# Kernel tuning notes

Measured on AMD Instinct MI355X. Metric: run time of the kernel, lower is better.

The kernel has to match this reference:

```python
import jax, jax.numpy as jnp
import numpy as np

DIM, HEADS, WH, WW, NPROMPT, NW, BATCH = 384, 12, 7, 7, 5, 64, 32
N = WH * WW + NPROMPT  # 54


def _make_rel_index():
    ch, cw = np.meshgrid(np.arange(WH), np.arange(WW), indexing='ij')
    coords = np.stack([ch, cw]).reshape(2, -1)  # [2, 49]
    rel = coords[:, :, None] - coords[:, None, :]  # [2,49,49]
    rel = rel.transpose(1, 2, 0)
    rel[:, :, 0] += WH - 1
    rel[:, :, 1] += WW - 1
    rel[:, :, 0] *= 2 * WW - 1
    return rel.sum(-1).astype(np.int32)  # [49,49]


def setup_inputs() -> dict:
    key = jax.random.key(0)
    ks = jax.random.split(key, 7)
    B_ = BATCH * NW
    x = jax.random.normal(ks[0], (B_, N, DIM), jnp.float32)
    # 0/-inf style shifted-window mask; random floats exercise the same math
    mask = jnp.where(jax.random.uniform(ks[1], (NW, WH * WW, WH * WW)) > 0.8,
                     jnp.float32(-100.0), jnp.float32(0.0))
    qkv_w = 0.02 * jax.random.normal(ks[2], (3 * DIM, DIM), jnp.float32)
    qkv_b = 0.02 * jax.random.normal(ks[3], (3 * DIM,), jnp.float32)
    proj_w = 0.02 * jax.random.normal(ks[4], (DIM, DIM), jnp.float32)
    proj_b = 0.02 * jax.random.normal(ks[5], (DIM,), jnp.float32)
    rpb_table = 0.02 * jax.random.normal(ks[6], ((2 * WH - 1) * (2 * WW - 1), HEADS), jnp.float32)
    rel_index = jnp.asarray(_make_rel_index())
    return {"x": x, "mask": mask, "qkv_w": qkv_w, "qkv_b": qkv_b,
            "proj_w": proj_w, "proj_b": proj_b, "rpb_table": rpb_table,
            "rel_index": rel_index}


def reference(x, mask, qkv_w, qkv_b, proj_w, proj_b, rpb_table, rel_index):
    B_, n, C = x.shape
    hd = C // HEADS
    scale = hd ** -0.5
    qkv = (x @ qkv_w.T + qkv_b).reshape(B_, n, 3, HEADS, hd)
    qkv = jnp.moveaxis(qkv, 2, 0)  # [3, B_, n, H, hd]
    q, k, v = qkv[0], qkv[1], qkv[2]  # [B_, n, H, hd]
    attn = jnp.einsum('bnhd,bmhd->bhnm', q * scale, k)  # [B_, H, n, n]
    nw2 = WH * WW
    bias = rpb_table[rel_index.reshape(-1)].reshape(nw2, nw2, HEADS)
    bias = jnp.transpose(bias, (2, 0, 1))  # [H, 49, 49]
    bias = jnp.pad(bias, ((0, 0), (NPROMPT, 0), (NPROMPT, 0)))  # [H, n, n]
    attn = attn + bias[None]
    nW = mask.shape[0]
    mask_p = jnp.pad(mask, ((0, 0), (NPROMPT, 0), (NPROMPT, 0)))  # [nW, n, n]
    attn = attn.reshape(B_ // nW, nW, HEADS, n, n) + mask_p[None, :, None]
    attn = jax.nn.softmax(attn.reshape(B_, HEADS, n, n), axis=-1)
    out = jnp.einsum('bhnm,bmhd->bnhd', attn, v).reshape(B_, n, C)
    return out @ proj_w.T + proj_b
```

## Files before the change

kernel.cpp:

```cpp
#include <hip/hip_runtime.h>

#define DIM 384
#define NH 12
#define NT 54
#define NWIN 64

typedef __attribute__((ext_vector_type(8))) short short8;
typedef __attribute__((ext_vector_type(4))) float f32x4;

__device__ __forceinline__ unsigned short f2bf(float f) {
  unsigned int u = __float_as_uint(f);
  u += 0x7fffu + ((u >> 16) & 1u);
  return (unsigned short)(u >> 16);
}
__device__ __forceinline__ float bf2f(unsigned short s) {
  return __uint_as_float((unsigned int)s << 16);
}

__global__ __launch_bounds__(256) void convert_x(
    const float* __restrict__ x, unsigned short* __restrict__ xb) {
  const size_t i8 = ((size_t)blockIdx.x * 256 + threadIdx.x) * 8;
  float4 fa = *(const float4*)&x[i8];
  float4 fb = *(const float4*)&x[i8 + 4];
  short8 s;
  s[0] = f2bf(fa.x); s[1] = f2bf(fa.y); s[2] = f2bf(fa.z); s[3] = f2bf(fa.w);
  s[4] = f2bf(fb.x); s[5] = f2bf(fb.y); s[6] = f2bf(fb.z); s[7] = f2bf(fb.w);
  *(short8*)&xb[i8] = s;
}

__global__ __launch_bounds__(256) void prep2_kernel(
    const float* __restrict__ qkv_w, const float* __restrict__ proj_w,
    const float* __restrict__ mask, const float* __restrict__ rpb,
    const int* __restrict__ rel,
    unsigned short* __restrict__ Wq, unsigned short* __restrict__ Wp,
    unsigned short* __restrict__ bmt) {
  int idx = blockIdx.x * 256 + threadIdx.x;
  if (idx < 1152 * 384) { Wq[idx] = f2bf(qkv_w[idx]); return; }
  idx -= 1152 * 384;
  if (idx < 384 * 384) { Wp[idx] = f2bf(proj_w[idx]); return; }
  idx -= 384 * 384;
  if (idx < NWIN * NH * 64 * 64) {
    int w = idx / (NH * 4096);
    int rem = idx - w * (NH * 4096);
    int h = rem >> 12, r = (rem >> 6) & 63, c = rem & 63;
    float v;
    if (r >= NT || c >= NT) v = -1e30f;
    else if (r >= 5 && c >= 5)
      v = rpb[rel[(r - 5) * 49 + (c - 5)] * NH + h] +
          mask[w * 2401 + (r - 5) * 49 + (c - 5)];
    else v = 0.0f;
    bmt[w * (NH * 4096) + rem] = f2bf(v);
  }
}

__global__ __launch_bounds__(256) void qkv_gemm2(
    const unsigned short* __restrict__ xb, const unsigned short* __restrict__ Wq,
    const float* __restrict__ qkv_b, unsigned short* __restrict__ QKVb) {
  __shared__ unsigned short As[128][72];
  __shared__ unsigned short Bs[128][72];
  const int tid = threadIdx.x;
  const int n0 = blockIdx.x * 128;
  const size_t m0 = (size_t)blockIdx.y * 128;
  const int wv = tid >> 6, ln = tid & 63, g = ln >> 4, lc = ln & 15;
  const int wr = (wv >> 1) * 64, wc = (wv & 1) * 64;
  f32x4 acc[4][4];
#pragma unroll
  for (int i = 0; i < 4; ++i)
#pragma unroll
    for (int j = 0; j < 4; ++j) acc[i][j] = (f32x4){0.f, 0.f, 0.f, 0.f};

  const int srow = tid >> 3, l8 = tid & 7;
  for (int kc = 0; kc < 6; ++kc) {
    const int k0 = kc * 64;
#pragma unroll
    for (int it = 0; it < 4; ++it) {
      const int r = srow + it * 32;
      *(short8*)&As[r][l8 * 8] =
          *(const short8*)&xb[(m0 + r) * 384 + k0 + l8 * 8];
      *(short8*)&Bs[r][l8 * 8] =
          *(const short8*)&Wq[(size_t)(n0 + r) * 384 + k0 + l8 * 8];
    }
    __syncthreads();
#pragma unroll
    for (int kk = 0; kk < 2; ++kk) {
      short8 af[4], bfr[4];
#pragma unroll
      for (int ms = 0; ms < 4; ++ms)
        af[ms] = *(const short8*)&As[wr + ms * 16 + lc][kk * 32 + g * 8];
#pragma unroll
      for (int ns = 0; ns < 4; ++ns)
        bfr[ns] = *(const short8*)&Bs[wc + ns * 16 + lc][kk * 32 + g * 8];
#pragma unroll
      for (int ms = 0; ms < 4; ++ms)
#pragma unroll
        for (int ns = 0; ns < 4; ++ns)
          acc[ms][ns] = __builtin_amdgcn_mfma_f32_16x16x32_bf16(
              af[ms], bfr[ns], acc[ms][ns], 0, 0, 0);
    }
    __syncthreads();
  }
  const float factor = (n0 < 384) ? 0.17677669529663687f : 1.0f;
#pragma unroll
  for (int ns = 0; ns < 4; ++ns) {
    const int n = n0 + wc + ns * 16 + lc;
    const float bias = qkv_b[n];
#pragma unroll
    for (int ms = 0; ms < 4; ++ms)
#pragma unroll
      for (int rr = 0; rr < 4; ++rr) {
        const size_t m = m0 + wr + ms * 16 + g * 4 + rr;
        QKVb[m * 1152 + n] = f2bf((acc[ms][ns][rr] + bias) * factor);
      }
  }
}

__global__ __launch_bounds__(256) void attn2_kernel(
    unsigned short* __restrict__ QKVb, const unsigned short* __restrict__ bmt) {
  __shared__ unsigned short Ps[NT][72];
  __shared__ unsigned short vT[32][72];
  const int h = blockIdx.x, b = blockIdx.y, tid = threadIdx.x;
  const int wv = tid >> 6, ln = tid & 63, g = ln >> 4, lc = ln & 15;
  const int m0 = wv * 16, wi = b & 63;
  const size_t base = (size_t)b * NT;
  const int arow = (m0 + lc < NT) ? (m0 + lc) : (NT - 1);

  for (int i = tid; i < 320; i += 256) {
    int d = i / 10, m = NT + (i - d * 10);
    vT[d][m] = 0;
  }

  const int vr = tid >> 2, vc = (tid & 3) * 8;
  short8 vv;
  if (tid < 216)
    vv = *(const short8*)&QKVb[(base + vr) * 1152 + 768 + h * 32 + vc];

  short8 a = *(const short8*)&QKVb[(base + arow) * 1152 + h * 32 + g * 8];
  const unsigned short* bmh = &bmt[(size_t)(wi * NH + h) << 12];
  f32x4 sac[4];
#pragma unroll
  for (int t = 0; t < 4; ++t) {
    const int kr = (t * 16 + lc < NT) ? (t * 16 + lc) : (NT - 1);
    short8 kb = *(const short8*)&QKVb[(base + kr) * 1152 + 384 + h * 32 + g * 8];
    f32x4 c0;
#pragma unroll
    for (int rr = 0; rr < 4; ++rr)
      c0[rr] = bf2f(bmh[(m0 + g * 4 + rr) * 64 + t * 16 + lc]);
    sac[t] = __builtin_amdgcn_mfma_f32_16x16x32_bf16(a, kb, c0, 0, 0, 0);
  }
  float rmax[4] = {-3.0e38f, -3.0e38f, -3.0e38f, -3.0e38f};
#pragma unroll
  for (int t = 0; t < 4; ++t)
#pragma unroll
    for (int rr = 0; rr < 4; ++rr) rmax[rr] = fmaxf(rmax[rr], sac[t][rr]);
#pragma unroll
  for (int rr = 0; rr < 4; ++rr)
#pragma unroll
    for (int off = 1; off < 16; off <<= 1)
      rmax[rr] = fmaxf(rmax[rr], __shfl_xor(rmax[rr], off));
  float rsum[4] = {0.f, 0.f, 0.f, 0.f};
#pragma unroll
  for (int t = 0; t < 4; ++t)
#pragma unroll
    for (int rr = 0; rr < 4; ++rr) {
      float p = __expf(sac[t][rr] - rmax[rr]);
      sac[t][rr] = p;
      rsum[rr] += p;
    }
#pragma unroll
  for (int rr = 0; rr < 4; ++rr) {
#pragma unroll
    for (int off = 1; off < 16; off <<= 1)
      rsum[rr] += __shfl_xor(rsum[rr], off);
    rsum[rr] = 1.0f / rsum[rr];
  }
#pragma unroll
  for (int t = 0; t < 4; ++t)
#pragma unroll
    for (int rr = 0; rr < 4; ++rr) {
      const int row = m0 + g * 4 + rr;
      if (row < NT) Ps[row][t * 16 + lc] = f2bf(sac[t][rr] * rsum[rr]);
    }
  if (tid < 216) {
#pragma unroll
    for (int j = 0; j < 8; ++j) vT[vc + j][vr] = (unsigned short)vv[j];
  }
  __syncthreads();
  f32x4 oac[2];
  oac[0] = (f32x4){0.f, 0.f, 0.f, 0.f};
  oac[1] = (f32x4){0.f, 0.f, 0.f, 0.f};
#pragma unroll
  for (int k2 = 0; k2 < 2; ++k2) {
    short8 pa = *(const short8*)&Ps[arow][k2 * 32 + g * 8];
#pragma unroll
    for (int tn = 0; tn < 2; ++tn) {
      short8 vb = *(const short8*)&vT[tn * 16 + lc][k2 * 32 + g * 8];
      oac[tn] = __builtin_amdgcn_mfma_f32_16x16x32_bf16(pa, vb, oac[tn], 0, 0, 0);
    }
  }
#pragma unroll
  for (int tn = 0; tn < 2; ++tn) {
    const int d = tn * 16 + lc;
#pragma unroll
    for (int rr = 0; rr < 4; ++rr) {
      const int m = m0 + g * 4 + rr;
      if (m < NT) QKVb[(base + m) * 1152 + h * 32 + d] = f2bf(oac[tn][rr]);
    }
  }
}

__global__ __launch_bounds__(256) void proj_kernel(
    const unsigned short* __restrict__ AO, const unsigned short* __restrict__ Wp,
    const float* __restrict__ proj_b, float* __restrict__ out, int lda) {
  __shared__ unsigned short As[128][72];
  __shared__ unsigned short Bs[128][72];
  const int tid = threadIdx.x;
  const size_t m0 = (size_t)blockIdx.x * 128;
  const int n0 = blockIdx.y * 128;
  const int wv = tid >> 6, ln = tid & 63, g = ln >> 4, lc = ln & 15;
  const int wr = (wv >> 1) * 64, wc = (wv & 1) * 64;
  f32x4 acc[4][4];
#pragma unroll
  for (int i = 0; i < 4; ++i)
#pragma unroll
    for (int j = 0; j < 4; ++j) acc[i][j] = (f32x4){0.f, 0.f, 0.f, 0.f};

  const int srow = tid >> 3, l8 = tid & 7;
  for (int kc = 0; kc < 6; ++kc) {
    const int k0 = kc * 64;
#pragma unroll
    for (int it = 0; it < 4; ++it) {
      const int r = srow + it * 32;
      *(short8*)&As[r][l8 * 8] =
          *(const short8*)&AO[(m0 + r) * (size_t)lda + k0 + l8 * 8];
      *(short8*)&Bs[r][l8 * 8] =
          *(const short8*)&Wp[(size_t)(n0 + r) * 384 + k0 + l8 * 8];
    }
    __syncthreads();
#pragma unroll
    for (int kk = 0; kk < 2; ++kk) {
      short8 af[4], bfr[4];
#pragma unroll
      for (int ms = 0; ms < 4; ++ms)
        af[ms] = *(const short8*)&As[wr + ms * 16 + lc][kk * 32 + g * 8];
#pragma unroll
      for (int ns = 0; ns < 4; ++ns)
        bfr[ns] = *(const short8*)&Bs[wc + ns * 16 + lc][kk * 32 + g * 8];
#pragma unroll
      for (int ms = 0; ms < 4; ++ms)
#pragma unroll
        for (int ns = 0; ns < 4; ++ns)
          acc[ms][ns] = __builtin_amdgcn_mfma_f32_16x16x32_bf16(
              af[ms], bfr[ns], acc[ms][ns], 0, 0, 0);
    }
    __syncthreads();
  }
#pragma unroll
  for (int ns = 0; ns < 4; ++ns) {
    const int n = n0 + wc + ns * 16 + lc;
    const float pb = proj_b[n];
#pragma unroll
    for (int ms = 0; ms < 4; ++ms)
#pragma unroll
      for (int rr = 0; rr < 4; ++rr) {
        const size_t m = m0 + wr + ms * 16 + g * 4 + rr;
        out[m * 384 + n] = acc[ms][ns][rr] + pb;
      }
  }
}

__global__ __launch_bounds__(256) void prep_kernel(
    const float* __restrict__ qkv_w, const float* __restrict__ proj_w,
    const float* __restrict__ mask, const float* __restrict__ rpb,
    const int* __restrict__ rel,
    unsigned short* __restrict__ Wq, unsigned short* __restrict__ Wp,
    float* __restrict__ bias_tab, float* __restrict__ maskp) {
  int idx = blockIdx.x * 256 + threadIdx.x;
  if (idx < 1152 * 384) { Wq[idx] = f2bf(qkv_w[idx]); return; }
  idx -= 1152 * 384;
  if (idx < 384 * 384) { Wp[idx] = f2bf(proj_w[idx]); return; }
  idx -= 384 * 384;
  if (idx < NH * 64 * 64) {
    int h = idx >> 12, r = (idx >> 6) & 63, c = idx & 63;
    float v;
    if (r >= NT || c >= NT) v = -1e30f;
    else if (r >= 5 && c >= 5) v = rpb[rel[(r - 5) * 49 + (c - 5)] * NH + h];
    else v = 0.0f;
    bias_tab[idx] = v;
    return;
  }
  idx -= NH * 64 * 64;
  if (idx < NWIN * 64 * 64) {
    int w = idx >> 12, r = (idx >> 6) & 63, c = idx & 63;
    float v = 0.0f;
    if (r >= 5 && r < NT && c >= 5 && c < NT)
      v = mask[w * 2401 + (r - 5) * 49 + (c - 5)];
    maskp[idx] = v;
  }
}

__global__ __launch_bounds__(256) void fused_attn(
    const float* __restrict__ x, const unsigned short* __restrict__ Wq,
    const float* __restrict__ qkv_b, const float* __restrict__ bias_tab,
    const float* __restrict__ maskp, unsigned short* __restrict__ AO) {
  __shared__ unsigned short xs[NT][392];
  __shared__ unsigned short qs[NT][40];
  __shared__ unsigned short ksm[NT][40];
  __shared__ unsigned short vT[32][72];
  __shared__ unsigned short Ps[NT][72];
  const int b = blockIdx.x;
  const int tid = threadIdx.x;
  const int wv = tid >> 6, ln = tid & 63;
  const int g = ln >> 4, lc = ln & 15;
  const int m0 = wv * 16;
  const int wi = b & 63;
  const float scale = 0.17677669529663687f;
  const float* xb = x + (size_t)b * (NT * DIM);
  for (int i = tid; i < NT * DIM / 4; i += 256) {
    float4 v = ((const float4*)xb)[i];
    int e = i * 4, r = e / DIM, c = e - r * DIM;
    unsigned short* p = &xs[r][c];
    p[0] = f2bf(v.x); p[1] = f2bf(v.y); p[2] = f2bf(v.z); p[3] = f2bf(v.w);
  }
  __syncthreads();
  const int arow = (m0 + lc < NT) ? (m0 + lc) : (NT - 1);
  for (int h = 0; h < NH; ++h) {
    f32x4 acc[6];
#pragma unroll
    for (int t = 0; t < 6; ++t) acc[t] = (f32x4){0.f, 0.f, 0.f, 0.f};
#pragma unroll 2
    for (int kk = 0; kk < 12; ++kk) {
      short8 a = *(const short8*)&xs[arow][kk * 32 + g * 8];
#pragma unroll
      for (int t = 0; t < 6; ++t) {
        const int sel = t >> 1;
        const int wrow = sel * 384 + h * 32 + (t & 1) * 16 + lc;
        short8 bfr = *(const short8*)&Wq[wrow * 384 + kk * 32 + g * 8];
        acc[t] = __builtin_amdgcn_mfma_f32_16x16x32_bf16(a, bfr, acc[t], 0, 0, 0);
      }
    }
#pragma unroll
    for (int t = 0; t < 6; ++t) {
      const int sel = t >> 1;
      const int d = (t & 1) * 16 + lc;
      const float bias = qkv_b[sel * 384 + h * 32 + d];
#pragma unroll
      for (int r = 0; r < 4; ++r) {
        const int m = m0 + g * 4 + r;
        float v = acc[t][r] + bias;
        if (sel == 2) vT[d][m] = f2bf(v);
        else if (m < NT) {
          if (sel == 0) qs[m][d] = f2bf(v * scale);
          else ksm[m][d] = f2bf(v);
        }
      }
    }
    __syncthreads();
    f32x4 sac[4];
    {
      short8 a = *(const short8*)&qs[arow][g * 8];
#pragma unroll
      for (int t = 0; t < 4; ++t) {
        const int kr = (t * 16 + lc < NT) ? (t * 16 + lc) : (NT - 1);
        short8 bfr = *(const short8*)&ksm[kr][g * 8];
        sac[t] = __builtin_amdgcn_mfma_f32_16x16x32_bf16(
            a, bfr, (f32x4){0.f, 0.f, 0.f, 0.f}, 0, 0, 0);
      }
    }
    const float* bt = bias_tab + h * 4096;
    const float* mp = maskp + wi * 4096;
    float sv[4][4];
    float rmax[4];
#pragma unroll
    for (int r = 0; r < 4; ++r) rmax[r] = -3.0e38f;
#pragma unroll
    for (int t = 0; t < 4; ++t) {
      const int col = t * 16 + lc;
#pragma unroll
      for (int r = 0; r < 4; ++r) {
        const int row = m0 + g * 4 + r;
        float s = sac[t][r] + bt[row * 64 + col] + mp[row * 64 + col];
        sv[t][r] = s;
        rmax[r] = fmaxf(rmax[r], s);
      }
    }
#pragma unroll
    for (int r = 0; r < 4; ++r)
#pragma unroll
      for (int off = 1; off < 16; off <<= 1)
        rmax[r] = fmaxf(rmax[r], __shfl_xor(rmax[r], off));
    float rsum[4] = {0.f, 0.f, 0.f, 0.f};
#pragma unroll
    for (int t = 0; t < 4; ++t)
#pragma unroll
      for (int r = 0; r < 4; ++r) {
        float p = __expf(sv[t][r] - rmax[r]);
        sv[t][r] = p;
        rsum[r] += p;
      }
#pragma unroll
    for (int r = 0; r < 4; ++r) {
#pragma unroll
      for (int off = 1; off < 16; off <<= 1)
        rsum[r] += __shfl_xor(rsum[r], off);
      rsum[r] = 1.0f / rsum[r];
    }
#pragma unroll
    for (int t = 0; t < 4; ++t) {
      const int col = t * 16 + lc;
#pragma unroll
      for (int r = 0; r < 4; ++r) {
        const int row = m0 + g * 4 + r;
        if (row < NT) Ps[row][col] = f2bf(sv[t][r] * rsum[r]);
      }
    }
    __syncthreads();
    f32x4 oac[2];
    oac[0] = (f32x4){0.f, 0.f, 0.f, 0.f};
    oac[1] = (f32x4){0.f, 0.f, 0.f, 0.f};
#pragma unroll
    for (int k2 = 0; k2 < 2; ++k2) {
      short8 a = *(const short8*)&Ps[arow][k2 * 32 + g * 8];
#pragma unroll
      for (int tn = 0; tn < 2; ++tn) {
        short8 bfr = *(const short8*)&vT[tn * 16 + lc][k2 * 32 + g * 8];
        oac[tn] = __builtin_amdgcn_mfma_f32_16x16x32_bf16(a, bfr, oac[tn], 0, 0, 0);
      }
    }
    unsigned short* aob = AO + (size_t)b * (NT * DIM) + h * 32;
#pragma unroll
    for (int tn = 0; tn < 2; ++tn) {
      const int d = tn * 16 + lc;
#pragma unroll
      for (int r = 0; r < 4; ++r) {
        const int m = m0 + g * 4 + r;
        if (m < NT) aob[m * DIM + d] = f2bf(oac[tn][r]);
      }
    }
    __syncthreads();
  }
}

extern "C" void kernel_launch(void* const* d_in, const int* in_sizes, int n_in,
                              void* d_out, int out_size, void* d_ws, size_t ws_size,
                              hipStream_t stream) {
  const float* x      = (const float*)d_in[0];
  const float* mask   = (const float*)d_in[1];
  const float* qkv_w  = (const float*)d_in[2];
  const float* qkv_b  = (const float*)d_in[3];
  const float* proj_w = (const float*)d_in[4];
  const float* proj_b = (const float*)d_in[5];
  const float* rpb    = (const float*)d_in[6];
  const int*   rel    = (const int*)d_in[7];
  float* out = (float*)d_out;

  const size_t M = 110592;
  const size_t QKV_ELEMS = M * 1152;
  const size_t WQ_ELEMS = 1152 * 384, WP_ELEMS = 384 * 384;
  const size_t BMT_ELEMS = (size_t)NWIN * NH * 4096;
  const size_t need = (QKV_ELEMS + WQ_ELEMS + WP_ELEMS + BMT_ELEMS) * 2;

  if (ws_size >= need) {
    unsigned short* QKVb = (unsigned short*)d_ws;
    unsigned short* Wq   = QKVb + QKV_ELEMS;
    unsigned short* Wp   = Wq + WQ_ELEMS;
    unsigned short* bmt  = Wp + WP_ELEMS;
    unsigned short* xb = (unsigned short*)d_out;

    convert_x<<<20736, 256, 0, stream>>>(x, xb);
    prep2_kernel<<<14592, 256, 0, stream>>>(qkv_w, proj_w, mask, rpb, rel,
                                            Wq, Wp, bmt);
    qkv_gemm2<<<dim3(9, 864), 256, 0, stream>>>(xb, Wq, qkv_b, QKVb);
    attn2_kernel<<<dim3(NH, 2048), 256, 0, stream>>>(QKVb, bmt);
    proj_kernel<<<dim3(864, 3), 256, 0, stream>>>(QKVb, Wp, proj_b, out, 1152);
  } else {
    unsigned short* Wq = (unsigned short*)d_ws;
    unsigned short* Wp = Wq + 442368;
    float* bias_tab = (float*)(Wp + 147456);
    float* maskp = bias_tab + 12 * 64 * 64;
    unsigned short* AO = (unsigned short*)(maskp + 64 * 64 * 64);
    prep_kernel<<<3520, 256, 0, stream>>>(qkv_w, proj_w, mask, rpb, rel,
                                          Wq, Wp, bias_tab, maskp);
    fused_attn<<<2048, 256, 0, stream>>>(x, Wq, qkv_b, bias_tab, maskp, AO);
    proj_kernel<<<dim3(864, 3), 256, 0, stream>>>(AO, Wp, proj_b, out, 384);
  }
}
```

Before: 458.8 us.

## Remap block indices for XCD-local L2 reuse and transpose bias-mask table

Flattens the grids of the QKV GEMM, attention and projection kernels and remaps block IDs so that consecutive blocks dispatched to the same XCD (id mod 8) work on contiguous row tiles or windows. This aims to keep A-tiles and per-window QKV data in that XCD's L2 instead of spreading them across all eight. The bias/mask table is also stored transposed, so each lane fetches its four bias values with one 8-byte load instead of four scattered 2-byte loads. The remap assumes round-robin XCD dispatch and grid sizes that divide evenly.

Result: faster. 436.4 us (-4.9%).

```diff
diff --git a/kernel.cpp b/kernel.cpp
--- a/kernel.cpp
+++ b/kernel.cpp
@@ -49,7 +49,7 @@
       v = rpb[rel[(r - 5) * 49 + (c - 5)] * NH + h] +
           mask[w * 2401 + (r - 5) * 49 + (c - 5)];
     else v = 0.0f;
-    bmt[w * (NH * 4096) + rem] = f2bf(v);
+    bmt[w * (NH * 4096) + (h << 12) + (c << 6) + r] = f2bf(v);
   }
 }
 
@@ -58,9 +58,11 @@
     const float* __restrict__ qkv_b, unsigned short* __restrict__ QKVb) {
   __shared__ unsigned short As[128][72];
   __shared__ unsigned short Bs[128][72];
+  const int s = blockIdx.x;
+  const int xcd = s & 7, slot = s >> 3;
+  const size_t m0 = (size_t)(xcd * 108 + slot / 9) * 128;
+  const int n0 = (slot % 9) * 128;
   const int tid = threadIdx.x;
-  const int n0 = blockIdx.x * 128;
-  const size_t m0 = (size_t)blockIdx.y * 128;
   const int wv = tid >> 6, ln = tid & 63, g = ln >> 4, lc = ln & 15;
   const int wr = (wv >> 1) * 64, wc = (wv & 1) * 64;
   f32x4 acc[4][4];
@@ -118,7 +120,11 @@
     unsigned short* __restrict__ QKVb, const unsigned short* __restrict__ bmt) {
   __shared__ unsigned short Ps[NT][72];
   __shared__ unsigned short vT[32][72];
-  const int h = blockIdx.x, b = blockIdx.y, tid = threadIdx.x;
+  const int s = blockIdx.x;
+  const int xcd = s & 7, slot = s >> 3;
+  const int b = xcd * 256 + slot / 12;
+  const int h = slot - 12 * (slot / 12);
+  const int tid = threadIdx.x;
   const int wv = tid >> 6, ln = tid & 63, g = ln >> 4, lc = ln & 15;
   const int m0 = wv * 16, wi = b & 63;
   const size_t base = (size_t)b * NT;
@@ -136,15 +142,19 @@
 
   short8 a = *(const short8*)&QKVb[(base + arow) * 1152 + h * 32 + g * 8];
   const unsigned short* bmh = &bmt[(size_t)(wi * NH + h) << 12];
+  const int row0 = m0 + g * 4;
   f32x4 sac[4];
 #pragma unroll
   for (int t = 0; t < 4; ++t) {
-    const int kr = (t * 16 + lc < NT) ? (t * 16 + lc) : (NT - 1);
+    const int col = t * 16 + lc;
+    const int kr = (col < NT) ? col : (NT - 1);
     short8 kb = *(const short8*)&QKVb[(base + kr) * 1152 + 384 + h * 32 + g * 8];
+    uint2 uu = *(const uint2*)&bmh[(col << 6) + row0];
     f32x4 c0;
-#pragma unroll
-    for (int rr = 0; rr < 4; ++rr)
-      c0[rr] = bf2f(bmh[(m0 + g * 4 + rr) * 64 + t * 16 + lc]);
+    c0[0] = bf2f((unsigned short)(uu.x & 0xffffu));
+    c0[1] = bf2f((unsigned short)(uu.x >> 16));
+    c0[2] = bf2f((unsigned short)(uu.y & 0xffffu));
+    c0[3] = bf2f((unsigned short)(uu.y >> 16));
     sac[t] = __builtin_amdgcn_mfma_f32_16x16x32_bf16(a, kb, c0, 0, 0, 0);
   }
   float rmax[4] = {-3.0e38f, -3.0e38f, -3.0e38f, -3.0e38f};
@@ -177,7 +187,7 @@
   for (int t = 0; t < 4; ++t)
 #pragma unroll
     for (int rr = 0; rr < 4; ++rr) {
-      const int row = m0 + g * 4 + rr;
+      const int row = row0 + rr;
       if (row < NT) Ps[row][t * 16 + lc] = f2bf(sac[t][rr] * rsum[rr]);
     }
   if (tid < 216) {
@@ -213,9 +223,11 @@
     const float* __restrict__ proj_b, float* __restrict__ out, int lda) {
   __shared__ unsigned short As[128][72];
   __shared__ unsigned short Bs[128][72];
+  const int s = blockIdx.x;
+  const int xcd = s & 7, slot = s >> 3;
+  const size_t m0 = (size_t)(xcd * 108 + slot / 3) * 128;
+  const int n0 = (slot % 3) * 128;
   const int tid = threadIdx.x;
-  const size_t m0 = (size_t)blockIdx.x * 128;
-  const int n0 = blockIdx.y * 128;
   const int wv = tid >> 6, ln = tid & 63, g = ln >> 4, lc = ln & 15;
   const int wr = (wv >> 1) * 64, wc = (wv & 1) * 64;
   f32x4 acc[4][4];
@@ -469,9 +481,9 @@
     convert_x<<<20736, 256, 0, stream>>>(x, xb);
     prep2_kernel<<<14592, 256, 0, stream>>>(qkv_w, proj_w, mask, rpb, rel,
                                             Wq, Wp, bmt);
-    qkv_gemm2<<<dim3(9, 864), 256, 0, stream>>>(xb, Wq, qkv_b, QKVb);
-    attn2_kernel<<<dim3(NH, 2048), 256, 0, stream>>>(QKVb, bmt);
-    proj_kernel<<<dim3(864, 3), 256, 0, stream>>>(QKVb, Wp, proj_b, out, 1152);
+    qkv_gemm2<<<7776, 256, 0, stream>>>(xb, Wq, qkv_b, QKVb);
+    attn2_kernel<<<24576, 256, 0, stream>>>(QKVb, bmt);
+    proj_kernel<<<2592, 256, 0, stream>>>(QKVb, Wp, proj_b, out, 1152);
   } else {
     unsigned short* Wq = (unsigned short*)d_ws;
     unsigned short* Wp = Wq + 442368;
@@ -481,6 +493,6 @@
     prep_kernel<<<3520, 256, 0, stream>>>(qkv_w, proj_w, mask, rpb, rel,
                                           Wq, Wp, bias_tab, maskp);
     fused_attn<<<2048, 256, 0, stream>>>(x, Wq, qkv_b, bias_tab, maskp, AO);
-    proj_kernel<<<dim3(864, 3), 256, 0, stream>>>(AO, Wp, proj_b, out, 384);
-  }
-}
+    proj_kernel<<<2592, 256, 0, stream>>>(AO, Wp, proj_b, out, 384);
+  }
+}
```
